# Optimization experiments

Measured on AMD Instinct MI355X. Metric: run time of the kernel, lower is better.

The kernel has to match this reference:

```python
import jax, jax.numpy as jnp
import numpy as np

N_NODES = 100000
N_EDGES = 3200000
IN_C, HID_C, OUT_C = 128, 64, 64


def setup_inputs() -> dict:
    key = jax.random.key(0)
    k = jax.random.split(key, 6)
    x = jax.random.normal(k[0], (N_NODES, IN_C), dtype=jnp.float32)
    edge_index = jax.random.randint(k[1], (2, N_EDGES), 0, N_NODES, dtype=jnp.int64)
    edge_weight = jax.random.uniform(k[2], (N_EDGES,), dtype=jnp.float32)
    W1 = jax.random.normal(k[3], (IN_C, HID_C), dtype=jnp.float32) * (1.0 / np.sqrt(IN_C))
    b1 = jnp.zeros((HID_C,), dtype=jnp.float32)
    W2 = jax.random.normal(k[4], (HID_C, OUT_C), dtype=jnp.float32) * (1.0 / np.sqrt(HID_C))
    b2 = jnp.zeros((OUT_C,), dtype=jnp.float32)
    return {"x": x, "edge_index": edge_index, "edge_weight": edge_weight,
            "W1": W1, "b1": b1, "W2": W2, "b2": b2}


def _gcn_norm(edge_index, edge_weight, num_nodes, dtype):
    # PyG GCNConv default: add self-loops (weight 1), symmetric normalization
    loop = jnp.arange(num_nodes, dtype=edge_index.dtype)
    row = jnp.concatenate([edge_index[0], loop])  # sources
    col = jnp.concatenate([edge_index[1], loop])  # targets (aggregation dim)
    w = jnp.concatenate([edge_weight.astype(dtype), jnp.ones((num_nodes,), dtype)])
    deg = jax.ops.segment_sum(w, col, num_segments=num_nodes)
    deg_inv_sqrt = jnp.where(deg > 0, jax.lax.rsqrt(deg), jnp.zeros((), dtype))
    norm = deg_inv_sqrt[row] * w * deg_inv_sqrt[col]
    return row, col, norm


def _gcn_conv(h, row, col, norm, W, b, num_nodes):
    h = h @ W                      # [N, C_out]
    msg = h[row] * norm[:, None]   # gather over sources, scale by edge norm
    out = jax.ops.segment_sum(msg, col, num_segments=num_nodes)  # scatter-add to targets
    return out + b


def reference(x, edge_index, edge_weight, W1, b1, W2, b2):
    num_nodes = x.shape[0]
    row, col, norm = _gcn_norm(edge_index, edge_weight, num_nodes, x.dtype)
    h = _gcn_conv(x, row, col, norm, W1, b1, num_nodes)
    h = jax.nn.relu(h)
    return _gcn_conv(h, row, col, norm, W2, b2, num_nodes)
```

## Files before the change

### kernel.cpp

```cpp
#include <hip/hip_runtime.h>
#include <hip/hip_bf16.h>

#define N_NODES 100000
#define N_EDGES 3200000
#define IN_C 128
#define HID_C 64
#define OUT_C 64

#define NBUCKET 196
#define SC_EDGES 4096
#define SC_GRID 782
#define CAP 18432

struct EdgeRec { int s; float v; };

typedef float f32x2 __attribute__((ext_vector_type(2)));
typedef float f32x4 __attribute__((ext_vector_type(4)));
typedef short bf16x8 __attribute__((ext_vector_type(8)));
union F8 { uint4 u; bf16x8 f; };

__device__ __forceinline__ unsigned pack_bf16(float lo, float hi) {
    unsigned short l = __hip_bfloat16_raw(__float2bfloat16(lo)).x;
    unsigned short h = __hip_bfloat16_raw(__float2bfloat16(hi)).x;
    return ((unsigned)h << 16) | l;
}
__device__ __forceinline__ float bf_lo(unsigned u) {
    union { unsigned u; float f; } c; c.u = u << 16; return c.f;
}
__device__ __forceinline__ float bf_hi(unsigned u) {
    union { unsigned u; float f; } c; c.u = u & 0xffff0000u; return c.f;
}
__device__ __forceinline__ f32x2 bfp(unsigned u) {
    union { unsigned u; float f; } lo, hi;
    lo.u = u << 16; hi.u = u & 0xffff0000u;
    f32x2 r; r.x = lo.f; r.y = hi.f; return r;
}
__device__ __forceinline__ void pk_fma(f32x2& acc, f32x2 a, f32x2 w) {
    asm("v_pk_fma_f32 %0, %1, %2, %0" : "+v"(acc) : "v"(a), "v"(w));
}
__device__ __forceinline__ void edge_acc(f32x2* acc2, uint4 u, float w) {
    f32x2 wv; wv.x = w; wv.y = w;
    pk_fma(acc2[0], bfp(u.x), wv);
    pk_fma(acc2[1], bfp(u.y), wv);
    pk_fma(acc2[2], bfp(u.z), wv);
    pk_fma(acc2[3], bfp(u.w), wv);
}
__device__ __forceinline__ unsigned cvt_pk_bf16(float lo, float hi) {
    unsigned r;
    asm("v_cvt_pk_bf16_f32 %0, %1, %2" : "=v"(r) : "v"(lo), "v"(hi));
    return r;
}
__device__ __forceinline__ void split_frag(const float* f, uint4& hi4, uint4& lo4) {
    unsigned hi[4], lo[4];
    #pragma unroll
    for (int p = 0; p < 4; ++p) {
        hi[p] = cvt_pk_bf16(f[2 * p], f[2 * p + 1]);
        float r0 = f[2 * p]     - bf_lo(hi[p]);
        float r1 = f[2 * p + 1] - bf_hi(hi[p]);
        lo[p] = cvt_pk_bf16(r0, r1);
    }
    hi4 = make_uint4(hi[0], hi[1], hi[2], hi[3]);
    lo4 = make_uint4(lo[0], lo[1], lo[2], lo[3]);
}

__global__ __launch_bounds__(256) void scatter_coarse(const int* __restrict__ ei,
                                                      const float* __restrict__ ew,
                                                      int* __restrict__ gcursor,
                                                      uint2* __restrict__ tmp) {
    __shared__ int hist[256];
    __shared__ int scan[256];
    __shared__ int lcur[256];
    __shared__ int adj[256];
    __shared__ uint2 rec[SC_EDGES];
    __shared__ unsigned char bk[SC_EDGES];
    int tid = threadIdx.x;
    hist[tid] = 0;
    __syncthreads();
    int base = blockIdx.x * SC_EDGES;
    unsigned ys[16];
    float    ws[16];
    int      bs[16];
    for (int i = 0; i < 16; ++i) {
        int e = base + i * 256 + tid;
        if (e < N_EDGES) {
            int t = ei[N_EDGES + e];
            bs[i] = t >> 9;
            ys[i] = (unsigned)ei[e] | ((unsigned)(t & 511) << 17);
            ws[i] = ew[e];
            atomicAdd(&hist[bs[i]], 1);
        } else bs[i] = -1;
    }
    __syncthreads();
    int v = hist[tid];
    scan[tid] = v;
    __syncthreads();
    for (int off = 1; off < 256; off <<= 1) {
        int t = scan[tid];
        int add = (tid >= off) ? scan[tid - off] : 0;
        __syncthreads();
        scan[tid] = t + add;
        __syncthreads();
    }
    int excl = scan[tid] - v;
    int gb = (v > 0) ? atomicAdd(&gcursor[tid], v) : 0;
    lcur[tid] = excl;
    adj[tid] = tid * CAP + gb - excl;
    __syncthreads();
    for (int i = 0; i < 16; ++i) {
        if (bs[i] >= 0) {
            int j = atomicAdd(&lcur[bs[i]], 1);
            rec[j] = make_uint2(__float_as_uint(ws[i]), ys[i]);
            bk[j] = (unsigned char)bs[i];
        }
    }
    __syncthreads();
    int count = N_EDGES - base;
    if (count > SC_EDGES) count = SC_EDGES;
    for (int j = tid; j < count; j += 256) {
        int b = bk[j];
        tmp[adj[b] + j] = rec[j];
    }
}

__global__ __launch_bounds__(256) void bucket_scan(const int* __restrict__ gcnt,
                                                   int* __restrict__ start) {
    __shared__ int s[256];
    int tid = threadIdx.x;
    int v = gcnt[tid];
    s[tid] = v;
    __syncthreads();
    for (int off = 1; off < 256; off <<= 1) {
        int t = s[tid];
        int add = (tid >= off) ? s[tid - off] : 0;
        __syncthreads();
        s[tid] = t + add;
        __syncthreads();
    }
    start[tid] = s[tid] - v;
    if (tid == 255) start[256] = s[255];
}

__global__ __launch_bounds__(512) void fine_sort(const int* __restrict__ start,
                                                 const uint2* __restrict__ tmpPad,
                                                 int* __restrict__ rowptr,
                                                 float* __restrict__ dis,
                                                 EdgeRec* __restrict__ ed) {
    __shared__ int   cnt[512];
    __shared__ float wdeg[512];
    __shared__ int   s[512];
    int tid = threadIdx.x;
    int nodeBase = blockIdx.x << 9;
    int bb = start[blockIdx.x];
    int nEdge = start[blockIdx.x + 1] - bb;
    const uint2* tb = tmpPad + (size_t)blockIdx.x * CAP;
    cnt[tid] = 0;
    wdeg[tid] = 0.f;
    __syncthreads();
    for (int e = tid; e < nEdge; e += 512) {
        uint2 r = tb[e];
        int l = (r.y >> 17) & 511;
        atomicAdd(&cnt[l], 1);
        atomicAdd(&wdeg[l], __uint_as_float(r.x));
    }
    __syncthreads();
    int v = cnt[tid];
    s[tid] = v;
    __syncthreads();
    for (int off = 1; off < 512; off <<= 1) {
        int t = s[tid];
        int add = (tid >= off) ? s[tid - off] : 0;
        __syncthreads();
        s[tid] = t + add;
        __syncthreads();
    }
    int excl = s[tid] - v;
    int node = nodeBase + tid;
    if (node < N_NODES) {
        rowptr[node] = bb + excl;
        dis[node] = rsqrtf(wdeg[tid] + 1.0f);
    }
    if (node == N_NODES) rowptr[N_NODES] = N_EDGES;
    cnt[tid] = excl;
    __syncthreads();
    for (int e = tid; e < nEdge; e += 512) {
        uint2 r = tb[e];
        int l = (r.y >> 17) & 511;
        int p = atomicAdd(&cnt[l], 1);
        EdgeRec o;
        o.s = (int)(r.y & 0x1FFFFu);
        o.v = __uint_as_float(r.x);
        ed[bb + p] = o;
    }
}

template<int K>
__global__ __launch_bounds__(256) void mm_mfma(const float* __restrict__ X,
                                               const float* __restrict__ W,
                                               const float* __restrict__ dis,
                                               unsigned* __restrict__ h) {
    constexpr int NKS = K / 32;
    int wv = threadIdx.x >> 6;
    int l  = threadIdx.x & 63;
    int lr = l & 15;
    int kr = l >> 4;
    int col = wv * 16 + lr;
    F8 bhi[NKS], blo[NKS];
    #pragma unroll
    for (int ks = 0; ks < NKS; ++ks) {
        const float* wp = W + (ks * 32 + kr * 8) * 64 + col;
        float f[8];
        #pragma unroll
        for (int j = 0; j < 8; ++j) f[j] = wp[j * 64];
        split_frag(f, bhi[ks].u, blo[ks].u);
    }
    for (int t = blockIdx.x; t < N_NODES / 16; t += gridDim.x) {
        int row0 = t * 16;
        f32x4 acc = {0.f, 0.f, 0.f, 0.f};
        #pragma unroll
        for (int ks = 0; ks < NKS; ++ks) {
            const float4* xp = (const float4*)(X + (size_t)(row0 + lr) * K + ks * 32 + kr * 8);
            float4 fa = xp[0], fb = xp[1];
            float f[8] = {fa.x, fa.y, fa.z, fa.w, fb.x, fb.y, fb.z, fb.w};
            F8 ahi, alo;
            split_frag(f, ahi.u, alo.u);
            acc = __builtin_amdgcn_mfma_f32_16x16x32_bf16(ahi.f, bhi[ks].f, acc, 0, 0, 0);
            acc = __builtin_amdgcn_mfma_f32_16x16x32_bf16(ahi.f, blo[ks].f, acc, 0, 0, 0);
            acc = __builtin_amdgcn_mfma_f32_16x16x32_bf16(alo.f, bhi[ks].f, acc, 0, 0, 0);
        }
        int rbase = row0 + kr * 4;
        float v0 = acc[0] * dis[rbase + 0];
        float v1 = acc[1] * dis[rbase + 1];
        float v2 = acc[2] * dis[rbase + 2];
        float v3 = acc[3] * dis[rbase + 3];
        float o0 = __shfl_xor(v0, 1, 64);
        float o1 = __shfl_xor(v1, 1, 64);
        float o2 = __shfl_xor(v2, 1, 64);
        float o3 = __shfl_xor(v3, 1, 64);
        if ((lr & 1) == 0) {
            int ci = col >> 1;
            h[(rbase + 0) * 32 + ci] = pack_bf16(v0, o0);
            h[(rbase + 1) * 32 + ci] = pack_bf16(v1, o1);
            h[(rbase + 2) * 32 + ci] = pack_bf16(v2, o2);
            h[(rbase + 3) * 32 + ci] = pack_bf16(v3, o3);
        }
    }
}

__global__ __launch_bounds__(256, 8) void agg_kernel(const int* __restrict__ rowptr,
                                                     const EdgeRec* __restrict__ ed,
                                                     const unsigned* __restrict__ h,
                                                     const float* __restrict__ dis,
                                                     const float* __restrict__ b,
                                                     float* __restrict__ out,
                                                     int relu) {
    int node = blockIdx.x * 4 + (threadIdx.x >> 6);
    int lane = threadIdx.x & 63;
    int g = lane >> 3;
    int cl = lane & 7;
    int beg = rowptr[node];
    int end = rowptr[node + 1];
    const uint4* h16 = (const uint4*)h;
    const char*  hb  = (const char*)h + (size_t)cl * 16;
    float d  = dis[node];
    uint4 us = h16[(size_t)node * 8 + cl];
    f32x2 acc2[4];
    acc2[0] = 0.f; acc2[1] = 0.f; acc2[2] = 0.f; acc2[3] = 0.f;
    int n = end - beg;
    int nb = (n + 31) >> 5;
    int nm1 = n - 1;
    uint2 q0, q1, q2, q3;
    if (nb > 0) {
        q0 = *(const uint2*)(ed + beg + min(g,      nm1));
        q1 = *(const uint2*)(ed + beg + min(g + 8,  nm1));
        q2 = *(const uint2*)(ed + beg + min(g + 16, nm1));
        q3 = *(const uint2*)(ed + beg + min(g + 24, nm1));
        for (int bt = 0; bt < nb; ++bt) {
            int ob = (bt << 5) + g;
            float w0 = (ob      < n) ? __uint_as_float(q0.y) : 0.f;
            float w1 = (ob + 8  < n) ? __uint_as_float(q1.y) : 0.f;
            float w2 = (ob + 16 < n) ? __uint_as_float(q2.y) : 0.f;
            float w3 = (ob + 24 < n) ? __uint_as_float(q3.y) : 0.f;
            uint4 u0 = *(const uint4*)(hb + ((size_t)(unsigned)q0.x << 7));
            uint4 u1 = *(const uint4*)(hb + ((size_t)(unsigned)q1.x << 7));
            uint4 u2 = *(const uint4*)(hb + ((size_t)(unsigned)q2.x << 7));
            uint4 u3 = *(const uint4*)(hb + ((size_t)(unsigned)q3.x << 7));
            if (bt + 1 < nb) {
                int on = ob + 32;
                q0 = *(const uint2*)(ed + beg + min(on,      nm1));
                q1 = *(const uint2*)(ed + beg + min(on + 8,  nm1));
                q2 = *(const uint2*)(ed + beg + min(on + 16, nm1));
                q3 = *(const uint2*)(ed + beg + min(on + 24, nm1));
            }
            edge_acc(acc2, u0, w0);
            edge_acc(acc2, u1, w1);
            edge_acc(acc2, u2, w2);
            edge_acc(acc2, u3, w3);
        }
    }
    float acc[8] = { acc2[0].x, acc2[0].y, acc2[1].x, acc2[1].y,
                     acc2[2].x, acc2[2].y, acc2[3].x, acc2[3].y };
    #pragma unroll
    for (int kk = 0; kk < 8; ++kk) {
        acc[kk] += __shfl_xor(acc[kk], 8, 64);
        acc[kk] += __shfl_xor(acc[kk], 16, 64);
        acc[kk] += __shfl_xor(acc[kk], 32, 64);
    }
    if (g == 0) {
        float hs[8] = { bf_lo(us.x), bf_hi(us.x), bf_lo(us.y), bf_hi(us.y),
                        bf_lo(us.z), bf_hi(us.z), bf_lo(us.w), bf_hi(us.w) };
        const float4* b4 = (const float4*)b;
        float4 bv0 = b4[cl * 2], bv1 = b4[cl * 2 + 1];
        float4 v0, v1;
        v0.x = d * (acc[0] + hs[0]) + bv0.x;
        v0.y = d * (acc[1] + hs[1]) + bv0.y;
        v0.z = d * (acc[2] + hs[2]) + bv0.z;
        v0.w = d * (acc[3] + hs[3]) + bv0.w;
        v1.x = d * (acc[4] + hs[4]) + bv1.x;
        v1.y = d * (acc[5] + hs[5]) + bv1.y;
        v1.z = d * (acc[6] + hs[6]) + bv1.z;
        v1.w = d * (acc[7] + hs[7]) + bv1.w;
        if (relu) {
            v0.x = fmaxf(v0.x, 0.f); v0.y = fmaxf(v0.y, 0.f);
            v0.z = fmaxf(v0.z, 0.f); v0.w = fmaxf(v0.w, 0.f);
            v1.x = fmaxf(v1.x, 0.f); v1.y = fmaxf(v1.y, 0.f);
            v1.z = fmaxf(v1.z, 0.f); v1.w = fmaxf(v1.w, 0.f);
        }
        float4* o4 = (float4*)out;
        o4[node * 16 + cl * 2]     = v0;
        o4[node * 16 + cl * 2 + 1] = v1;
    }
}

extern "C" void kernel_launch(void* const* d_in, const int* in_sizes, int n_in,
                              void* d_out, int out_size, void* d_ws, size_t ws_size,
                              hipStream_t stream) {
    const float* x  = (const float*)d_in[0];
    const int*   ei = (const int*)d_in[1];
    const float* ew = (const float*)d_in[2];
    const float* W1 = (const float*)d_in[3];
    const float* b1 = (const float*)d_in[4];
    const float* W2 = (const float*)d_in[5];
    const float* b2 = (const float*)d_in[6];
    float* out = (float*)d_out;

    char* p = (char*)d_ws;
    auto carve = [&](size_t bytes) { char* r = p; p += (bytes + 255) & ~(size_t)255; return r; };
    float*    dis     = (float*)carve(N_NODES * 4);
    int*      rowptr  = (int*)carve((N_NODES + 1) * 4);
    int*      start   = (int*)carve(257 * 4);
    int*      gcursor = (int*)carve(256 * 4);
    EdgeRec*  ed      = (EdgeRec*)carve((size_t)N_EDGES * 8);
    size_t    r2sz    = (size_t)NBUCKET * CAP * 8;
    size_t    hasz    = (size_t)N_NODES * 64 * 6;
    char*     r2      = carve(r2sz > hasz ? r2sz : hasz);
    uint2*    tmpPad  = (uint2*)r2;
    unsigned* h       = (unsigned*)r2;
    float*    a       = (float*)(r2 + (size_t)N_NODES * 64 * 2);

    hipMemsetAsync(gcursor, 0, 256 * sizeof(int), stream);
    scatter_coarse<<<SC_GRID, 256, 0, stream>>>(ei, ew, gcursor, tmpPad);
    bucket_scan<<<1, 256, 0, stream>>>(gcursor, start);
    fine_sort<<<NBUCKET, 512, 0, stream>>>(start, tmpPad, rowptr, dis, ed);

    mm_mfma<IN_C><<<1250, 256, 0, stream>>>(x, W1, dis, h);
    agg_kernel<<<N_NODES / 4, 256, 0, stream>>>(rowptr, ed, h, dis, b1, a, 1);

    mm_mfma<HID_C><<<1250, 256, 0, stream>>>(a, W2, dis, h);
    agg_kernel<<<N_NODES / 4, 256, 0, stream>>>(rowptr, ed, h, dis, b2, out, 0);
}
```

Measured before the change: 352.6 us.

## Overlap first-layer GEMM with coarse edge scatter in one fused launch

The first X@W1 GEMM no longer depends on the degree normalization. It is computed unscaled into an fp32 buffer by extra blocks appended to the coarse scatter kernel, so it runs concurrently with the edge bucketing. A new scalepack kernel then applies the per-node degree scale and packs to bf16 once fine_sort has produced it. This hides GEMM latency behind the memory-bound scatter, at the cost of an extra fp32 write/read of the hidden features. The fast path also needs a larger workspace and falls back to the old schedule otherwise.

```diff
diff --git a/kernel.cpp b/kernel.cpp
--- a/kernel.cpp
+++ b/kernel.cpp
@@ -11,6 +11,7 @@
 #define SC_EDGES 4096
 #define SC_GRID 782
 #define CAP 18432
+#define MM1_GRID (N_NODES / 16)
 
 struct EdgeRec { int s; float v; };
 
@@ -63,16 +64,13 @@
     lo4 = make_uint4(lo[0], lo[1], lo[2], lo[3]);
 }
 
-__global__ __launch_bounds__(256) void scatter_coarse(const int* __restrict__ ei,
-                                                      const float* __restrict__ ew,
-                                                      int* __restrict__ gcursor,
-                                                      uint2* __restrict__ tmp) {
-    __shared__ int hist[256];
-    __shared__ int scan[256];
-    __shared__ int lcur[256];
-    __shared__ int adj[256];
-    __shared__ uint2 rec[SC_EDGES];
-    __shared__ unsigned char bk[SC_EDGES];
+__device__ __forceinline__ void scatter_body(const int* __restrict__ ei,
+                                             const float* __restrict__ ew,
+                                             int* __restrict__ gcursor,
+                                             uint2* __restrict__ tmp,
+                                             int* hist, int* scn, int* lcur,
+                                             int* adj, uint2* rec,
+                                             unsigned char* bk) {
     int tid = threadIdx.x;
     hist[tid] = 0;
     __syncthreads();
@@ -92,16 +90,16 @@
     }
     __syncthreads();
     int v = hist[tid];
-    scan[tid] = v;
+    scn[tid] = v;
     __syncthreads();
     for (int off = 1; off < 256; off <<= 1) {
-        int t = scan[tid];
-        int add = (tid >= off) ? scan[tid - off] : 0;
-        __syncthreads();
-        scan[tid] = t + add;
-        __syncthreads();
-    }
-    int excl = scan[tid] - v;
+        int t = scn[tid];
+        int add = (tid >= off) ? scn[tid - off] : 0;
+        __syncthreads();
+        scn[tid] = t + add;
+        __syncthreads();
+    }
+    int excl = scn[tid] - v;
     int gb = (v > 0) ? atomicAdd(&gcursor[tid], v) : 0;
     lcur[tid] = excl;
     adj[tid] = tid * CAP + gb - excl;
@@ -122,75 +120,100 @@
     }
 }
 
-__global__ __launch_bounds__(256) void bucket_scan(const int* __restrict__ gcnt,
-                                                   int* __restrict__ start) {
-    __shared__ int s[256];
-    int tid = threadIdx.x;
-    int v = gcnt[tid];
-    s[tid] = v;
-    __syncthreads();
-    for (int off = 1; off < 256; off <<= 1) {
-        int t = s[tid];
-        int add = (tid >= off) ? s[tid - off] : 0;
-        __syncthreads();
-        s[tid] = t + add;
-        __syncthreads();
-    }
-    start[tid] = s[tid] - v;
-    if (tid == 255) start[256] = s[255];
-}
-
-__global__ __launch_bounds__(512) void fine_sort(const int* __restrict__ start,
-                                                 const uint2* __restrict__ tmpPad,
-                                                 int* __restrict__ rowptr,
-                                                 float* __restrict__ dis,
-                                                 EdgeRec* __restrict__ ed) {
-    __shared__ int   cnt[512];
-    __shared__ float wdeg[512];
-    __shared__ int   s[512];
-    int tid = threadIdx.x;
-    int nodeBase = blockIdx.x << 9;
-    int bb = start[blockIdx.x];
-    int nEdge = start[blockIdx.x + 1] - bb;
-    const uint2* tb = tmpPad + (size_t)blockIdx.x * CAP;
-    cnt[tid] = 0;
-    wdeg[tid] = 0.f;
-    __syncthreads();
-    for (int e = tid; e < nEdge; e += 512) {
-        uint2 r = tb[e];
-        int l = (r.y >> 17) & 511;
-        atomicAdd(&cnt[l], 1);
-        atomicAdd(&wdeg[l], __uint_as_float(r.x));
-    }
-    __syncthreads();
-    int v = cnt[tid];
-    s[tid] = v;
-    __syncthreads();
-    for (int off = 1; off < 512; off <<= 1) {
-        int t = s[tid];
-        int add = (tid >= off) ? s[tid - off] : 0;
-        __syncthreads();
-        s[tid] = t + add;
-        __syncthreads();
-    }
-    int excl = s[tid] - v;
-    int node = nodeBase + tid;
-    if (node < N_NODES) {
-        rowptr[node] = bb + excl;
-        dis[node] = rsqrtf(wdeg[tid] + 1.0f);
-    }
-    if (node == N_NODES) rowptr[N_NODES] = N_EDGES;
-    cnt[tid] = excl;
-    __syncthreads();
-    for (int e = tid; e < nEdge; e += 512) {
-        uint2 r = tb[e];
-        int l = (r.y >> 17) & 511;
-        int p = atomicAdd(&cnt[l], 1);
-        EdgeRec o;
-        o.s = (int)(r.y & 0x1FFFFu);
-        o.v = __uint_as_float(r.x);
-        ed[bb + p] = o;
-    }
+template<int K>
+__device__ __forceinline__ void mm_tile_raw(int tile,
+                                            const float* __restrict__ X,
+                                            const float* __restrict__ W,
+                                            float* __restrict__ hf) {
+    constexpr int NKS = K / 32;
+    int wv = threadIdx.x >> 6;
+    int l  = threadIdx.x & 63;
+    int lr = l & 15;
+    int kr = l >> 4;
+    int col = wv * 16 + lr;
+    int row0 = tile * 16;
+    const float* xbase = X + (size_t)(row0 + lr) * K + kr * 8;
+    float4 xa[NKS], xb[NKS];
+    #pragma unroll
+    for (int ks = 0; ks < NKS; ++ks) {
+        const float4* xp = (const float4*)(xbase + ks * 32);
+        xa[ks] = xp[0];
+        xb[ks] = xp[1];
+    }
+    F8 bhi[NKS], blo[NKS];
+    #pragma unroll
+    for (int ks = 0; ks < NKS; ++ks) {
+        const float* wp = W + (ks * 32 + kr * 8) * 64 + col;
+        float f[8];
+        #pragma unroll
+        for (int j = 0; j < 8; ++j) f[j] = wp[j * 64];
+        split_frag(f, bhi[ks].u, blo[ks].u);
+    }
+    f32x4 acc = {0.f, 0.f, 0.f, 0.f};
+    #pragma unroll
+    for (int ks = 0; ks < NKS; ++ks) {
+        float f[8] = {xa[ks].x, xa[ks].y, xa[ks].z, xa[ks].w,
+                      xb[ks].x, xb[ks].y, xb[ks].z, xb[ks].w};
+        F8 ahi, alo;
+        split_frag(f, ahi.u, alo.u);
+        acc = __builtin_amdgcn_mfma_f32_16x16x32_bf16(ahi.f, bhi[ks].f, acc, 0, 0, 0);
+        acc = __builtin_amdgcn_mfma_f32_16x16x32_bf16(ahi.f, blo[ks].f, acc, 0, 0, 0);
+        acc = __builtin_amdgcn_mfma_f32_16x16x32_bf16(alo.f, bhi[ks].f, acc, 0, 0, 0);
+    }
+    int rbase = row0 + kr * 4;
+    hf[(size_t)(rbase + 0) * 64 + col] = acc[0];
+    hf[(size_t)(rbase + 1) * 64 + col] = acc[1];
+    hf[(size_t)(rbase + 2) * 64 + col] = acc[2];
+    hf[(size_t)(rbase + 3) * 64 + col] = acc[3];
+}
+
+__global__ __launch_bounds__(256) void fused_scatter_mm1(const int* __restrict__ ei,
+                                                         const float* __restrict__ ew,
+                                                         int* __restrict__ gcursor,
+                                                         uint2* __restrict__ tmp,
+                                                         const float* __restrict__ x,
+                                                         const float* __restrict__ W1,
+                                                         float* __restrict__ hf) {
+    __shared__ int hist[256];
+    __shared__ int scn[256];
+    __shared__ int lcur[256];
+    __shared__ int adj[256];
+    __shared__ uint2 rec[SC_EDGES];
+    __shared__ unsigned char bk[SC_EDGES];
+    if (blockIdx.x >= SC_GRID) {
+        mm_tile_raw<IN_C>(blockIdx.x - SC_GRID, x, W1, hf);
+        return;
+    }
+    scatter_body(ei, ew, gcursor, tmp, hist, scn, lcur, adj, rec, bk);
+}
+
+__global__ __launch_bounds__(256) void scatter_coarse(const int* __restrict__ ei,
+                                                      const float* __restrict__ ew,
+                                                      int* __restrict__ gcursor,
+                                                      uint2* __restrict__ tmp) {
+    __shared__ int hist[256];
+    __shared__ int scn[256];
+    __shared__ int lcur[256];
+    __shared__ int adj[256];
+    __shared__ uint2 rec[SC_EDGES];
+    __shared__ unsigned char bk[SC_EDGES];
+    scatter_body(ei, ew, gcursor, tmp, hist, scn, lcur, adj, rec, bk);
+}
+
+__global__ __launch_bounds__(256) void scalepack(const float* __restrict__ hf,
+                                                 const float* __restrict__ dis,
+                                                 unsigned* __restrict__ h) {
+    int t = blockIdx.x * 256 + threadIdx.x;
+    int row = t >> 3, c8 = (t & 7) * 8;
+    const float4* p4 = (const float4*)(hf + (size_t)row * 64 + c8);
+    float4 f0 = p4[0], f1 = p4[1];
+    float d = dis[row];
+    uint4 o;
+    o.x = pack_bf16(d * f0.x, d * f0.y);
+    o.y = pack_bf16(d * f0.z, d * f0.w);
+    o.z = pack_bf16(d * f1.x, d * f1.y);
+    o.w = pack_bf16(d * f1.z, d * f1.w);
+    ((uint4*)h)[(size_t)row * 8 + (t & 7)] = o;
 }
 
 template<int K>
@@ -243,6 +266,77 @@
             h[(rbase + 2) * 32 + ci] = pack_bf16(v2, o2);
             h[(rbase + 3) * 32 + ci] = pack_bf16(v3, o3);
         }
+    }
+}
+
+__global__ __launch_bounds__(256) void bucket_scan(const int* __restrict__ gcnt,
+                                                   int* __restrict__ start) {
+    __shared__ int s[256];
+    int tid = threadIdx.x;
+    int v = gcnt[tid];
+    s[tid] = v;
+    __syncthreads();
+    for (int off = 1; off < 256; off <<= 1) {
+        int t = s[tid];
+        int add = (tid >= off) ? s[tid - off] : 0;
+        __syncthreads();
+        s[tid] = t + add;
+        __syncthreads();
+    }
+    start[tid] = s[tid] - v;
+    if (tid == 255) start[256] = s[255];
+}
+
+__global__ __launch_bounds__(512) void fine_sort(const int* __restrict__ start,
+                                                 const uint2* __restrict__ tmpPad,
+                                                 int* __restrict__ rowptr,
+                                                 float* __restrict__ dis,
+                                                 EdgeRec* __restrict__ ed) {
+    __shared__ int   cnt[512];
+    __shared__ float wdeg[512];
+    __shared__ int   s[512];
+    int tid = threadIdx.x;
+    int nodeBase = blockIdx.x << 9;
+    int bb = start[blockIdx.x];
+    int nEdge = start[blockIdx.x + 1] - bb;
+    const uint2* tb = tmpPad + (size_t)blockIdx.x * CAP;
+    cnt[tid] = 0;
+    wdeg[tid] = 0.f;
+    __syncthreads();
+    for (int e = tid; e < nEdge; e += 512) {
+        uint2 r = tb[e];
+        int l = (r.y >> 17) & 511;
+        atomicAdd(&cnt[l], 1);
+        atomicAdd(&wdeg[l], __uint_as_float(r.x));
+    }
+    __syncthreads();
+    int v = cnt[tid];
+    s[tid] = v;
+    __syncthreads();
+    for (int off = 1; off < 512; off <<= 1) {
+        int t = s[tid];
+        int add = (tid >= off) ? s[tid - off] : 0;
+        __syncthreads();
+        s[tid] = t + add;
+        __syncthreads();
+    }
+    int excl = s[tid] - v;
+    int node = nodeBase + tid;
+    if (node < N_NODES) {
+        rowptr[node] = bb + excl;
+        dis[node] = rsqrtf(wdeg[tid] + 1.0f);
+    }
+    if (node == N_NODES) rowptr[N_NODES] = N_EDGES;
+    cnt[tid] = excl;
+    __syncthreads();
+    for (int e = tid; e < nEdge; e += 512) {
+        uint2 r = tb[e];
+        int l = (r.y >> 17) & 511;
+        int p = atomicAdd(&cnt[l], 1);
+        EdgeRec o;
+        o.s = (int)(r.y & 0x1FFFFu);
+        o.v = __uint_as_float(r.x);
+        ed[bb + p] = o;
     }
 }
 
@@ -345,26 +439,45 @@
 
     char* p = (char*)d_ws;
     auto carve = [&](size_t bytes) { char* r = p; p += (bytes + 255) & ~(size_t)255; return r; };
-    float*    dis     = (float*)carve(N_NODES * 4);
     int*      rowptr  = (int*)carve((N_NODES + 1) * 4);
     int*      start   = (int*)carve(257 * 4);
     int*      gcursor = (int*)carve(256 * 4);
+    float*    dis     = (float*)carve(N_NODES * 4);
     EdgeRec*  ed      = (EdgeRec*)carve((size_t)N_EDGES * 8);
-    size_t    r2sz    = (size_t)NBUCKET * CAP * 8;
-    size_t    hasz    = (size_t)N_NODES * 64 * 6;
-    char*     r2      = carve(r2sz > hasz ? r2sz : hasz);
-    uint2*    tmpPad  = (uint2*)r2;
-    unsigned* h       = (unsigned*)r2;
-    float*    a       = (float*)(r2 + (size_t)N_NODES * 64 * 2);
-
-    hipMemsetAsync(gcursor, 0, 256 * sizeof(int), stream);
-    scatter_coarse<<<SC_GRID, 256, 0, stream>>>(ei, ew, gcursor, tmpPad);
-    bucket_scan<<<1, 256, 0, stream>>>(gcursor, start);
-    fine_sort<<<NBUCKET, 512, 0, stream>>>(start, tmpPad, rowptr, dis, ed);
-
-    mm_mfma<IN_C><<<1250, 256, 0, stream>>>(x, W1, dis, h);
-    agg_kernel<<<N_NODES / 4, 256, 0, stream>>>(rowptr, ed, h, dis, b1, a, 1);
-
-    mm_mfma<HID_C><<<1250, 256, 0, stream>>>(a, W2, dis, h);
-    agg_kernel<<<N_NODES / 4, 256, 0, stream>>>(rowptr, ed, h, dis, b2, out, 0);
-}
+    unsigned* h       = (unsigned*)carve((size_t)N_NODES * 64 * 2);
+
+    size_t tmpsz = (size_t)NBUCKET * CAP * 8;
+    size_t hfsz  = (size_t)N_NODES * 64 * 4;
+    size_t used  = (size_t)(p - (char*)d_ws);
+    bool fast = ws_size >= used + hfsz + tmpsz + 512;
+
+    if (fast) {
+        float* hf     = (float*)carve(hfsz);
+        uint2* tmpPad = (uint2*)carve(tmpsz);
+        float* a      = hf;
+
+        hipMemsetAsync(gcursor, 0, 256 * sizeof(int), stream);
+        fused_scatter_mm1<<<SC_GRID + MM1_GRID, 256, 0, stream>>>(ei, ew, gcursor,
+                                                                  tmpPad, x, W1, hf);
+        bucket_scan<<<1, 256, 0, stream>>>(gcursor, start);
+        fine_sort<<<NBUCKET, 512, 0, stream>>>(start, tmpPad, rowptr, dis, ed);
+        scalepack<<<N_NODES * 8 / 256, 256, 0, stream>>>(hf, dis, h);
+        agg_kernel<<<N_NODES / 4, 256, 0, stream>>>(rowptr, ed, h, dis, b1, a, 1);
+        mm_mfma<HID_C><<<1250, 256, 0, stream>>>(a, W2, dis, h);
+        agg_kernel<<<N_NODES / 4, 256, 0, stream>>>(rowptr, ed, h, dis, b2, out, 0);
+    } else {
+        size_t asz = (size_t)N_NODES * 64 * 4;
+        char*  r2  = carve(tmpsz > asz ? tmpsz : asz);
+        uint2* tmpPad = (uint2*)r2;
+        float* a      = (float*)r2;
+
+        hipMemsetAsync(gcursor, 0, 256 * sizeof(int), stream);
+        scatter_coarse<<<SC_GRID, 256, 0, stream>>>(ei, ew, gcursor, tmpPad);
+        bucket_scan<<<1, 256, 0, stream>>>(gcursor, start);
+        fine_sort<<<NBUCKET, 512, 0, stream>>>(start, tmpPad, rowptr, dis, ed);
+        mm_mfma<IN_C><<<1250, 256, 0, stream>>>(x, W1, dis, h);
+        agg_kernel<<<N_NODES / 4, 256, 0, stream>>>(rowptr, ed, h, dis, b1, a, 1);
+        mm_mfma<HID_C><<<1250, 256, 0, stream>>>(a, W2, dis, h);
+        agg_kernel<<<N_NODES / 4, 256, 0, stream>>>(rowptr, ed, h, dis, b2, out, 0);
+    }
+}
```

Measured after the change: 357.1 us. No clear change (+1.3%).
